# Kernel tuning notes

Hardware: AMD Instinct MI355X
Metric: run time of the kernel (lower is better)

Reference implementation:

```python
import jax, jax.numpy as jnp
import numpy as np

ALPHA = 0.2          # leaky relu negative slope
SCALE_ATT = 1.0
NEG_MASK = -9e15


def setup_inputs() -> dict:
    key = jax.random.key(0)
    k1, k2, k3, k4 = jax.random.split(key, 4)
    B, N, Din, Dout = 32, 1024, 256, 256
    h = jax.random.normal(k1, (B, N, Din), dtype=jnp.float32)
    adj = jax.random.randint(k2, (B, N, N), 0, 2, dtype=jnp.int32)
    W = jax.random.normal(k3, (Dout, Din), dtype=jnp.float32) * (1.0 / np.sqrt(Din))
    b = jnp.zeros((Dout,), dtype=jnp.float32)
    a = jax.random.normal(k4, (2 * Dout,), dtype=jnp.float32) * 0.1
    return {"h": h, "adj": adj, "W": W, "b": b, "a": a}


def reference(h, adj, W, b, a):
    # z: [B, N, Dout]
    z = jnp.einsum('bnd,od->bno', h, W) + b
    Dout = z.shape[-1]
    a1, a2 = a[:Dout], a[Dout:]
    # a^T [z_i || z_j] = a1.z_i + a2.z_j  (same math as the N^2 concat)
    s1 = jnp.einsum('bnd,d->bn', z, a1)  # source score per node
    s2 = jnp.einsum('bnd,d->bn', z, a2)  # target score per node
    e = jax.nn.leaky_relu(s1[:, :, None] + s2[:, None, :], negative_slope=ALPHA)
    e = jnp.where(adj > 0, e, NEG_MASK) * SCALE_ATT
    attention = jax.nn.softmax(e, axis=-1)   # [B, N, N]
    # dropout p=0 / eval mode: no-op
    h_prime = jnp.einsum('bij,bjd->bid', attention, z)
    return jax.nn.elu(h_prime)
```

## Files before the change

kernel.cpp:

```cpp
#include <hip/hip_runtime.h>
#include <math.h>

#define LRELU_ALPHA 0.2f
#define NEG_MASK_V -9000000000000000.0f

typedef __attribute__((ext_vector_type(8))) short short8;
typedef __attribute__((ext_vector_type(4))) float floatx4;
typedef __attribute__((ext_vector_type(8))) unsigned short u16x8;
typedef __attribute__((ext_vector_type(4))) unsigned short u16x4;

__device__ __forceinline__ unsigned short f2bf(float x) {
  union { float f; unsigned u; } v; v.f = x;
  unsigned r = v.u + 0x7fff + ((v.u >> 16) & 1);
  return (unsigned short)(r >> 16);
}

__device__ __forceinline__ unsigned cvt_pk_bf16(float lo, float hi) {
  unsigned r;
  asm("v_cvt_pk_bf16_f32 %0, %1, %2" : "=v"(r) : "v"(lo), "v"(hi));
  return r;
}

__global__ __launch_bounds__(256) void prep_kernel(
    const float* __restrict__ W, const float* __restrict__ b,
    const float* __restrict__ a, unsigned short* __restrict__ Wf,
    float* __restrict__ u1, float* __restrict__ u2, float* __restrict__ cst)
{
  const int t = threadIdx.x;
  if (blockIdx.x == 0) {
    float a1s = 0.f, a2s = 0.f;
    #pragma unroll 4
    for (int o = 0; o < 256; ++o) {
      const float w = W[o * 256 + t];
      a1s = fmaf(w, a[o], a1s);
      a2s = fmaf(w, a[256 + o], a2s);
    }
    u1[t] = a1s; u2[t] = a2s;
    if (t < 64) {
      float p1 = 0.f, p2 = 0.f;
      #pragma unroll
      for (int q = 0; q < 4; ++q) {
        const float bv = b[t + q * 64];
        p1 = fmaf(bv, a[t + q * 64], p1);
        p2 = fmaf(bv, a[256 + t + q * 64], p2);
      }
      #pragma unroll
      for (int off = 32; off > 0; off >>= 1) {
        p1 += __shfl_xor(p1, off); p2 += __shfl_xor(p2, off);
      }
      if (t == 0) { cst[0] = p1; cst[1] = p2; }
    }
  } else {
    const int base = (blockIdx.x - 1) * 2048 + t * 8;
    const int o = base >> 8;
    const int k = base & 255;
    const int region = k >> 3;
    const float4 v0 = *(const float4*)&W[base];
    const float4 v1 = *(const float4*)&W[base + 4];
    u16x8 ov;
    ov[0] = f2bf(v0.x); ov[1] = f2bf(v0.y); ov[2] = f2bf(v0.z); ov[3] = f2bf(v0.w);
    ov[4] = f2bf(v1.x); ov[5] = f2bf(v1.y); ov[6] = f2bf(v1.z); ov[7] = f2bf(v1.w);
    *(u16x8*)&Wf[((size_t)region * 256 + o) * 8] = ov;
  }
}

__global__ __launch_bounds__(256) void sdot_kernel(
    const float* __restrict__ h, const float* __restrict__ u1,
    const float* __restrict__ u2, const float* __restrict__ cst,
    float* __restrict__ s1, float* __restrict__ s2)
{
  const int t = threadIdx.x, l = t & 63, w = t >> 6;
  const long row0 = (long)blockIdx.x * 64 + w * 16;
  const float4 u1v = *(const float4*)&u1[l * 4];
  const float4 u2v = *(const float4*)&u2[l * 4];
  const float c1 = cst[0], c2 = cst[1];
  #pragma unroll
  for (int r = 0; r < 16; ++r) {
    const float4 hv = *(const float4*)&h[(row0 + r) * 256 + l * 4];
    float d1 = hv.x * u1v.x + hv.y * u1v.y + hv.z * u1v.z + hv.w * u1v.w;
    float d2 = hv.x * u2v.x + hv.y * u2v.y + hv.z * u2v.z + hv.w * u2v.w;
    #pragma unroll
    for (int off = 32; off > 0; off >>= 1) {
      d1 += __shfl_xor(d1, off); d2 += __shfl_xor(d2, off);
    }
    if (l == 0) { s1[row0 + r] = d1 + c1; s2[row0 + r] = d2 + c2; }
  }
}

__global__ __launch_bounds__(256) void zmfma_kernel(
    const float* __restrict__ h, const unsigned short* __restrict__ Wf,
    const float* __restrict__ bias, unsigned short* __restrict__ zf)
{
  __shared__ unsigned short h_tile[2][64][72];

  const int t = threadIdx.x, l = t & 63, w = t >> 6;
  const int g = l >> 4;
  const int bi = blockIdx.x;
  const long row0 = (long)bi * 64;

  floatx4 acc[4][4];
  #pragma unroll
  for (int mf = 0; mf < 4; ++mf)
    #pragma unroll
    for (int nf = 0; nf < 4; ++nf) acc[mf][nf] = (floatx4)0.f;

  const int srow = t >> 4, scol = (t & 15) * 4;

  #pragma unroll
  for (int p = 0; p < 4; ++p) {
    const float4 hv = *(const float4*)&h[(row0 + p * 16 + srow) * 256 + scol];
    uint2 hb;
    hb.x = cvt_pk_bf16(hv.x, hv.y);
    hb.y = cvt_pk_bf16(hv.z, hv.w);
    *(uint2*)&h_tile[0][p * 16 + srow][scol] = hb;
  }
  __syncthreads();

  #pragma unroll
  for (int s = 0; s < 4; ++s) {
    if (s < 3) {
      const int k0n = (s + 1) * 64;
      #pragma unroll
      for (int p = 0; p < 4; ++p) {
        const float4 hv =
            *(const float4*)&h[(row0 + p * 16 + srow) * 256 + k0n + scol];
        uint2 hb;
        hb.x = cvt_pk_bf16(hv.x, hv.y);
        hb.y = cvt_pk_bf16(hv.z, hv.w);
        *(uint2*)&h_tile[(s + 1) & 1][p * 16 + srow][scol] = hb;
      }
    }

    short8 wf[2][4];
    #pragma unroll
    for (int kk = 0; kk < 2; ++kk)
      #pragma unroll
      for (int nf = 0; nf < 4; ++nf)
        wf[kk][nf] = *(const short8*)&Wf[
            ((size_t)(s * 8 + kk * 4 + g) * 256 + w * 64 + nf * 16 + (l & 15)) * 8];

    #pragma unroll
    for (int kk = 0; kk < 2; ++kk) {
      short8 af[4];
      #pragma unroll
      for (int mf = 0; mf < 4; ++mf)
        af[mf] = *(const short8*)&h_tile[s & 1][mf * 16 + (l & 15)][kk * 32 + g * 8];
      #pragma unroll
      for (int nf = 0; nf < 4; ++nf) {
        #pragma unroll
        for (int mf = 0; mf < 4; ++mf)
          acc[mf][nf] = __builtin_amdgcn_mfma_f32_16x16x32_bf16(
              af[mf], wf[kk][nf], acc[mf][nf], 0, 0, 0);
      }
    }
    if (s < 3) __syncthreads();
  }

  #pragma unroll
  for (int nf = 0; nf < 4; ++nf) {
    const int o = w * 64 + nf * 16 + (l & 15);
    const float bv = bias[o];
    #pragma unroll
    for (int mf = 0; mf < 4; ++mf) {
      const int jbase = mf * 16 + g * 4;
      const int kk = jbase >> 5;
      const int lg = (jbase >> 3) & 3;
      const int jq = jbase & 7;
      uint2 zv;
      zv.x = cvt_pk_bf16(acc[mf][nf][0] + bv, acc[mf][nf][1] + bv);
      zv.y = cvt_pk_bf16(acc[mf][nf][2] + bv, acc[mf][nf][3] + bv);
      *(uint2*)&zf[((size_t)bi * 8 + kk * 4 + lg) * 2048 + (size_t)o * 8 + jq] = zv;
    }
  }
}

__global__ __launch_bounds__(512, 4) void attn_kernel(
    const unsigned short* __restrict__ zf, const float* __restrict__ s1g,
    const float* __restrict__ s2g, const int* __restrict__ adj,
    float* __restrict__ out)
{
  __shared__ unsigned short p_lds[64][72];
  __shared__ float s2s[1024];
  __shared__ float s1s[64];
  __shared__ float sum_lds[64];

  const int t = threadIdx.x;
  const int l = t & 63;
  const int w = t >> 6;

  const int wg = blockIdx.x;
  const int sw = (wg & 7) * 64 + (wg >> 3);
  const int b = sw >> 4;
  const int i0 = (sw & 15) * 64;

  const int i_loc = t >> 3;
  const int jb = (t & 7) * 8;

  const size_t adj_base = (size_t)b * 1024 * 1024 + (size_t)(i0 + i_loc) * 1024 + jb;
  const size_t zf_batch = (size_t)b * 16 * 16384;
  const size_t zf_lane  = (size_t)(l >> 4) * 2048 + (size_t)(w * 32 + (l & 15)) * 8;

  if (t < 64) s1s[t] = s1g[b * 1024 + i0 + t];
  s2s[t] = s2g[b * 1024 + t];
  s2s[512 + t] = s2g[b * 1024 + 512 + t];

  floatx4 acc[4][2];
  #pragma unroll
  for (int mf = 0; mf < 4; ++mf) {
    acc[mf][0] = (floatx4)0.f;
    acc[mf][1] = (floatx4)0.f;
  }
  float sm = 0.f;

  int4 ac0 = *(const int4*)&adj[adj_base];
  int4 ac1 = *(const int4*)&adj[adj_base + 4];

  short8 vz[2][4];
  {
    const unsigned short* zp = zf + zf_batch + zf_lane;
    vz[0][0] = *(const short8*)(zp);
    vz[0][1] = *(const short8*)(zp + 128);
    vz[0][2] = *(const short8*)(zp + 8192);
    vz[0][3] = *(const short8*)(zp + 8320);
  }
  __syncthreads();
  const float s1v = s1s[i_loc];

  for (int jt2 = 0; jt2 < 1024; jt2 += 128) {
    #pragma unroll
    for (int ph = 0; ph < 2; ++ph) {
      const int jt = jt2 + ph * 64;

      const float4 s2a = *(const float4*)&s2s[jt + jb];
      const float4 s2b = *(const float4*)&s2s[jt + jb + 4];
      float e[8] = {s2a.x, s2a.y, s2a.z, s2a.w, s2b.x, s2b.y, s2b.z, s2b.w};
      const int am[8] = {ac0.x, ac0.y, ac0.z, ac0.w, ac1.x, ac1.y, ac1.z, ac1.w};
      #pragma unroll
      for (int q = 0; q < 8; ++q) {
        float x = s1v + e[q];
        x = fmaxf(x, LRELU_ALPHA * x);
        e[q] = am[q] > 0 ? x : NEG_MASK_V;
      }

      if (jt + 64 < 1024) {
        ac0 = *(const int4*)&adj[adj_base + jt + 64];
        ac1 = *(const int4*)&adj[adj_base + jt + 68];
        const unsigned short* zp =
            zf + zf_batch + (size_t)((jt >> 6) + 1) * 16384 + zf_lane;
        vz[ph ^ 1][0] = *(const short8*)(zp);
        vz[ph ^ 1][1] = *(const short8*)(zp + 128);
        vz[ph ^ 1][2] = *(const short8*)(zp + 8192);
        vz[ph ^ 1][3] = *(const short8*)(zp + 8320);
      }

      float p[8];
      #pragma unroll
      for (int q = 0; q < 8; ++q) { p[q] = __expf(e[q]); sm += p[q]; }
      uint4 pk;
      pk.x = cvt_pk_bf16(p[0], p[1]);
      pk.y = cvt_pk_bf16(p[2], p[3]);
      pk.z = cvt_pk_bf16(p[4], p[5]);
      pk.w = cvt_pk_bf16(p[6], p[7]);

      __syncthreads();
      *(uint4*)&p_lds[i_loc][jb] = pk;
      __syncthreads();

      #pragma unroll
      for (int kk = 0; kk < 2; ++kk) {
        #pragma unroll
        for (int mf = 0; mf < 4; ++mf) {
          const short8 af =
              *(const short8*)&p_lds[mf * 16 + (l & 15)][kk * 32 + (l >> 4) * 8];
          acc[mf][0] = __builtin_amdgcn_mfma_f32_16x16x32_bf16(
              af, vz[ph][kk * 2 + 0], acc[mf][0], 0, 0, 0);
          acc[mf][1] = __builtin_amdgcn_mfma_f32_16x16x32_bf16(
              af, vz[ph][kk * 2 + 1], acc[mf][1], 0, 0, 0);
        }
      }
    }
  }

  sm += __shfl_xor(sm, 1);
  sm += __shfl_xor(sm, 2);
  sm += __shfl_xor(sm, 4);
  if ((t & 7) == 0) sum_lds[i_loc] = sm;
  __syncthreads();

  const size_t obase = ((size_t)b * 1024 + i0) * 256 + w * 32;
  #pragma unroll
  for (int mf = 0; mf < 4; ++mf) {
    const int rbase = mf * 16 + ((l >> 4) << 2);
    #pragma unroll
    for (int rg = 0; rg < 4; ++rg) {
      const float inv = 1.0f / sum_lds[rbase + rg];
      #pragma unroll
      for (int nf = 0; nf < 2; ++nf) {
        float v = acc[mf][nf][rg] * inv;
        v = v > 0.f ? v : expm1f(v);
        out[obase + (size_t)(rbase + rg) * 256 + nf * 16 + (l & 15)] = v;
      }
    }
  }
}

extern "C" void kernel_launch(void* const* d_in, const int* in_sizes, int n_in,
                              void* d_out, int out_size, void* d_ws, size_t ws_size,
                              hipStream_t stream) {
  const float* h    = (const float*)d_in[0];
  const int*   adj  = (const int*)d_in[1];
  const float* W    = (const float*)d_in[2];
  const float* bias = (const float*)d_in[3];
  const float* a    = (const float*)d_in[4];
  float* out = (float*)d_out;

  unsigned short* zf = (unsigned short*)d_ws;
  float* s1  = (float*)((char*)d_ws + 16777216);
  float* s2  = (float*)((char*)d_ws + 16908288);
  float* u1  = (float*)((char*)d_ws + 17039360);
  float* u2  = (float*)((char*)d_ws + 17040384);
  float* cst = (float*)((char*)d_ws + 17041408);
  unsigned short* Wf = (unsigned short*)((char*)d_ws + 17825792);

  prep_kernel<<<dim3(33), dim3(256), 0, stream>>>(W, bias, a, Wf, u1, u2, cst);
  sdot_kernel<<<dim3(512), dim3(256), 0, stream>>>(h, u1, u2, cst, s1, s2);
  zmfma_kernel<<<dim3(512), dim3(256), 0, stream>>>(h, Wf, bias, zf);
  attn_kernel<<<dim3(512), dim3(512), 0, stream>>>(zf, s1, s2, adj, out);
}
```

Before: 76.04 us.

## Fuse score dot-products into projection GEMM and halve row tile

Drops the separate sdot kernel and computes the s1/s2 per-node scores inside the projection kernel. They are accumulated in fp32 from the same h loads already used to stage bf16 tiles, and reduced with 16-lane shuffles at the end. This stops h being read from memory a second time and removes one kernel launch. The row tile per block also drops from 64 to 32 with twice as many blocks, and the zf output indexing is remapped so two adjacent blocks fill one 64-row region. The cost is less W-fragment reuse per block, since each block now reloads Wf for only 32 rows.

```diff
diff --git a/kernel.cpp b/kernel.cpp
--- a/kernel.cpp
+++ b/kernel.cpp
@@ -64,55 +64,44 @@
   }
 }
 
-__global__ __launch_bounds__(256) void sdot_kernel(
-    const float* __restrict__ h, const float* __restrict__ u1,
-    const float* __restrict__ u2, const float* __restrict__ cst,
-    float* __restrict__ s1, float* __restrict__ s2)
-{
-  const int t = threadIdx.x, l = t & 63, w = t >> 6;
-  const long row0 = (long)blockIdx.x * 64 + w * 16;
-  const float4 u1v = *(const float4*)&u1[l * 4];
-  const float4 u2v = *(const float4*)&u2[l * 4];
-  const float c1 = cst[0], c2 = cst[1];
-  #pragma unroll
-  for (int r = 0; r < 16; ++r) {
-    const float4 hv = *(const float4*)&h[(row0 + r) * 256 + l * 4];
-    float d1 = hv.x * u1v.x + hv.y * u1v.y + hv.z * u1v.z + hv.w * u1v.w;
-    float d2 = hv.x * u2v.x + hv.y * u2v.y + hv.z * u2v.z + hv.w * u2v.w;
-    #pragma unroll
-    for (int off = 32; off > 0; off >>= 1) {
-      d1 += __shfl_xor(d1, off); d2 += __shfl_xor(d2, off);
-    }
-    if (l == 0) { s1[row0 + r] = d1 + c1; s2[row0 + r] = d2 + c2; }
-  }
-}
-
 __global__ __launch_bounds__(256) void zmfma_kernel(
     const float* __restrict__ h, const unsigned short* __restrict__ Wf,
-    const float* __restrict__ bias, unsigned short* __restrict__ zf)
+    const float* __restrict__ bias, const float* __restrict__ u1,
+    const float* __restrict__ u2, const float* __restrict__ cst,
+    unsigned short* __restrict__ zf, float* __restrict__ s1,
+    float* __restrict__ s2)
 {
-  __shared__ unsigned short h_tile[2][64][72];
+  __shared__ unsigned short h_tile[2][32][72];
 
   const int t = threadIdx.x, l = t & 63, w = t >> 6;
   const int g = l >> 4;
   const int bi = blockIdx.x;
-  const long row0 = (long)bi * 64;
-
-  floatx4 acc[4][4];
-  #pragma unroll
-  for (int mf = 0; mf < 4; ++mf)
+  const long row0 = (long)bi * 32;
+
+  floatx4 acc[2][4];
+  #pragma unroll
+  for (int mf = 0; mf < 2; ++mf)
     #pragma unroll
     for (int nf = 0; nf < 4; ++nf) acc[mf][nf] = (floatx4)0.f;
 
+  float d1a[2] = {0.f, 0.f};
+  float d2a[2] = {0.f, 0.f};
+
   const int srow = t >> 4, scol = (t & 15) * 4;
 
-  #pragma unroll
-  for (int p = 0; p < 4; ++p) {
-    const float4 hv = *(const float4*)&h[(row0 + p * 16 + srow) * 256 + scol];
-    uint2 hb;
-    hb.x = cvt_pk_bf16(hv.x, hv.y);
-    hb.y = cvt_pk_bf16(hv.z, hv.w);
-    *(uint2*)&h_tile[0][p * 16 + srow][scol] = hb;
+  {
+    const float4 u1v = *(const float4*)&u1[scol];
+    const float4 u2v = *(const float4*)&u2[scol];
+    #pragma unroll
+    for (int p = 0; p < 2; ++p) {
+      const float4 hv = *(const float4*)&h[(row0 + p * 16 + srow) * 256 + scol];
+      d1a[p] = fmaf(hv.x, u1v.x, fmaf(hv.y, u1v.y, fmaf(hv.z, u1v.z, fmaf(hv.w, u1v.w, d1a[p]))));
+      d2a[p] = fmaf(hv.x, u2v.x, fmaf(hv.y, u2v.y, fmaf(hv.z, u2v.z, fmaf(hv.w, u2v.w, d2a[p]))));
+      uint2 hb;
+      hb.x = cvt_pk_bf16(hv.x, hv.y);
+      hb.y = cvt_pk_bf16(hv.z, hv.w);
+      *(uint2*)&h_tile[0][p * 16 + srow][scol] = hb;
+    }
   }
   __syncthreads();
 
@@ -120,10 +109,14 @@
   for (int s = 0; s < 4; ++s) {
     if (s < 3) {
       const int k0n = (s + 1) * 64;
-      #pragma unroll
-      for (int p = 0; p < 4; ++p) {
+      const float4 u1v = *(const float4*)&u1[k0n + scol];
+      const float4 u2v = *(const float4*)&u2[k0n + scol];
+      #pragma unroll
+      for (int p = 0; p < 2; ++p) {
         const float4 hv =
             *(const float4*)&h[(row0 + p * 16 + srow) * 256 + k0n + scol];
+        d1a[p] = fmaf(hv.x, u1v.x, fmaf(hv.y, u1v.y, fmaf(hv.z, u1v.z, fmaf(hv.w, u1v.w, d1a[p]))));
+        d2a[p] = fmaf(hv.x, u2v.x, fmaf(hv.y, u2v.y, fmaf(hv.z, u2v.z, fmaf(hv.w, u2v.w, d2a[p]))));
         uint2 hb;
         hb.x = cvt_pk_bf16(hv.x, hv.y);
         hb.y = cvt_pk_bf16(hv.z, hv.w);
@@ -141,19 +134,35 @@
 
     #pragma unroll
     for (int kk = 0; kk < 2; ++kk) {
-      short8 af[4];
-      #pragma unroll
-      for (int mf = 0; mf < 4; ++mf)
+      short8 af[2];
+      #pragma unroll
+      for (int mf = 0; mf < 2; ++mf)
         af[mf] = *(const short8*)&h_tile[s & 1][mf * 16 + (l & 15)][kk * 32 + g * 8];
       #pragma unroll
       for (int nf = 0; nf < 4; ++nf) {
         #pragma unroll
-        for (int mf = 0; mf < 4; ++mf)
+        for (int mf = 0; mf < 2; ++mf)
           acc[mf][nf] = __builtin_amdgcn_mfma_f32_16x16x32_bf16(
               af[mf], wf[kk][nf], acc[mf][nf], 0, 0, 0);
       }
     }
     if (s < 3) __syncthreads();
+  }
+
+  {
+    const float c1 = cst[0], c2 = cst[1];
+    #pragma unroll
+    for (int p = 0; p < 2; ++p) {
+      float d1 = d1a[p], d2 = d2a[p];
+      #pragma unroll
+      for (int off = 8; off > 0; off >>= 1) {
+        d1 += __shfl_xor(d1, off); d2 += __shfl_xor(d2, off);
+      }
+      if ((t & 15) == 0) {
+        const long row = row0 + p * 16 + srow;
+        s1[row] = d1 + c1; s2[row] = d2 + c2;
+      }
+    }
   }
 
   #pragma unroll
@@ -161,15 +170,13 @@
     const int o = w * 64 + nf * 16 + (l & 15);
     const float bv = bias[o];
     #pragma unroll
-    for (int mf = 0; mf < 4; ++mf) {
-      const int jbase = mf * 16 + g * 4;
-      const int kk = jbase >> 5;
-      const int lg = (jbase >> 3) & 3;
-      const int jq = jbase & 7;
+    for (int mf = 0; mf < 2; ++mf) {
+      const int region = (bi & 1) * 4 + mf * 2 + (g >> 1);
+      const int jq = (g & 1) * 4;
       uint2 zv;
       zv.x = cvt_pk_bf16(acc[mf][nf][0] + bv, acc[mf][nf][1] + bv);
       zv.y = cvt_pk_bf16(acc[mf][nf][2] + bv, acc[mf][nf][3] + bv);
-      *(uint2*)&zf[((size_t)bi * 8 + kk * 4 + lg) * 2048 + (size_t)o * 8 + jq] = zv;
+      *(uint2*)&zf[((size_t)(bi >> 1) * 8 + region) * 2048 + (size_t)o * 8 + jq] = zv;
     }
   }
 }
@@ -323,7 +330,6 @@
   unsigned short* Wf = (unsigned short*)((char*)d_ws + 17825792);
 
   prep_kernel<<<dim3(33), dim3(256), 0, stream>>>(W, bias, a, Wf, u1, u2, cst);
-  sdot_kernel<<<dim3(512), dim3(256), 0, stream>>>(h, u1, u2, cst, s1, s2);
-  zmfma_kernel<<<dim3(512), dim3(256), 0, stream>>>(h, Wf, bias, zf);
+  zmfma_kernel<<<dim3(1024), dim3(256), 0, stream>>>(h, Wf, bias, u1, u2, cst, zf, s1, s2);
   attn_kernel<<<dim3(512), dim3(512), 0, stream>>>(zf, s1, s2, adj, out);
 }
```

Measured after the change: 69.52 us. 1.09x faster.
